# Kernel tuning notes

Measured on AMD Instinct MI355X. Metric: run time of the kernel, lower is better.

Reference implementation:

```python
import jax, jax.numpy as jnp
import numpy as np

B, S, D, H, DH, DF = 8, 1024, 512, 8, 64, 2048
EPS = 1e-5


def layer_norm(x, g, b):
    mu = jnp.mean(x, axis=-1, keepdims=True)
    var = jnp.mean(jnp.square(x - mu), axis=-1, keepdims=True)
    return (x - mu) * jax.lax.rsqrt(var + EPS) * g + b


def rel_shift(x):
    # Transformer-XL relative shift: [b,h,q,k] -> shifted [b,h,q,k]
    b, h, q, k = x.shape
    x = jnp.pad(x, ((0, 0), (0, 0), (0, 0), (1, 0)))
    x = x.reshape(b, h, k + 1, q)[:, :, 1:, :].reshape(b, h, q, k)
    return x


def setup_inputs() -> dict:
    key = jax.random.key(0)
    ks = jax.random.split(key, 16)
    sc = 0.02
    inp = {
        'x': jax.random.normal(ks[0], (B, S, D), jnp.float32),
        'rel_positions': jax.random.normal(ks[1], (S, D), jnp.float32),
        'mask': jnp.triu(jnp.ones((S, S), jnp.bool_), k=1),  # True = masked (causal)
        'Wq': jax.random.normal(ks[2], (D, D), jnp.float32) * sc,
        'Wk': jax.random.normal(ks[3], (D, D), jnp.float32) * sc,
        'Wv': jax.random.normal(ks[4], (D, D), jnp.float32) * sc,
        'Wr': jax.random.normal(ks[5], (D, D), jnp.float32) * sc,
        'Wo': jax.random.normal(ks[6], (D, D), jnp.float32) * sc,
        'u_bias': jax.random.normal(ks[7], (H, DH), jnp.float32) * sc,
        'v_bias': jax.random.normal(ks[8], (H, DH), jnp.float32) * sc,
        'ln1_g': jnp.ones((D,), jnp.float32),
        'ln1_b': jnp.zeros((D,), jnp.float32),
        'W1': jax.random.normal(ks[9], (D, DF), jnp.float32) * sc,
        'b1': jnp.zeros((DF,), jnp.float32),
        'W2': jax.random.normal(ks[10], (DF, D), jnp.float32) * sc,
        'b2': jnp.zeros((D,), jnp.float32),
        'ln2_g': jnp.ones((D,), jnp.float32),
        'ln2_b': jnp.zeros((D,), jnp.float32),
    }
    return inp


def reference(x, rel_positions, mask, Wq, Wk, Wv, Wr, Wo, u_bias, v_bias,
              ln1_g, ln1_b, W1, b1, W2, b2, ln2_g, ln2_b):
    b, s, d = x.shape
    q = (x @ Wq).reshape(b, s, H, DH)
    k = (x @ Wk).reshape(b, s, H, DH)
    v = (x @ Wv).reshape(b, s, H, DH)
    r = (rel_positions @ Wr).reshape(s, H, DH)
    # content term (q + u) k^T and position term (q + v) r^T with rel-shift
    ac = jnp.einsum('bqhd,bkhd->bhqk', q + u_bias, k)
    bd = rel_shift(jnp.einsum('bqhd,khd->bhqk', q + v_bias, r))
    scores = (ac + bd) * (1.0 / np.sqrt(DH))
    scores = jnp.where(mask[None, None, :, :], jnp.asarray(-1e9, scores.dtype), scores)
    attn = jax.nn.softmax(scores, axis=-1)
    ctx = jnp.einsum('bhqk,bkhd->bqhd', attn, v).reshape(b, s, d) @ Wo
    h1 = layer_norm(x + ctx, ln1_g, ln1_b)
    ff = jax.nn.relu(h1 @ W1 + b1) @ W2 + b2
    out = layer_norm(h1 + ff, ln2_g, ln2_b)
    return out, attn
```

## Files before the change

kernel.cpp:

```cpp
#include <hip/hip_runtime.h>
#include <hip/hip_bf16.h>

typedef __hip_bfloat16 bf16;

#define NB 8
#define NS 1024
#define ND 512
#define NH 8
#define NDH 64
#define NDF 2048

typedef __attribute__((ext_vector_type(8))) short s16x8;
typedef __attribute__((ext_vector_type(4))) float f32x4;

__device__ __forceinline__ void storev(float* p, float v) { *p = v; }
__device__ __forceinline__ void storev(bf16* p, float v) { *p = __float2bfloat16(v); }
__device__ __forceinline__ short f2bf(float f) {
    bf16 h = __float2bfloat16(f);
    return *reinterpret_cast<short*>(&h);
}
__device__ __forceinline__ float bf2f(short s) {
    bf16 h = *reinterpret_cast<bf16*>(&s);
    return __bfloat162float(h);
}

__device__ __forceinline__ void gload_lds16(const short* g, short* l) {
    __builtin_amdgcn_global_load_lds(
        (const __attribute__((address_space(1))) unsigned int*)g,
        (__attribute__((address_space(3))) unsigned int*)l, 16, 0, 0);
}

__global__ __launch_bounds__(256) void cast2_kernel(
    const float4* __restrict__ inA, int n4a,
    const float4* __restrict__ inB, int n4b,
    short* __restrict__ outA, short* __restrict__ outB)
{
    int i = blockIdx.x * 256 + threadIdx.x;
    const float4* s; short* d; int j;
    if (i < n4a) { s = inA; d = outA; j = i; }
    else if (i < n4a + n4b) { s = inB; d = outB; j = i - n4a; }
    else return;
    float4 v = s[j];
    short4 o;
    o.x = f2bf(v.x); o.y = f2bf(v.y); o.z = f2bf(v.z); o.w = f2bf(v.w);
    *reinterpret_cast<short4*>(d + (size_t)j * 4) = o;
}

struct TP7 {
    const float* src[7];
    short* dst[7];
    int K[7];
    int N[7];
};

__global__ __launch_bounds__(256) void transpose_cast_all_kernel(TP7 p)
{
    __shared__ float t[32][33];
    const int z = blockIdx.z;
    const float* src = p.src[z];
    short* dst = p.dst[z];
    const int K = p.K[z], N = p.N[z];
    const int ntx = N >> 5;
    const int f = blockIdx.x;
    if (f >= ntx * (K >> 5)) return;
    const int n0 = (f % ntx) * 32, k0 = (f / ntx) * 32;
    const int tx = threadIdx.x & 31, ty = threadIdx.x >> 5;
#pragma unroll
    for (int i = 0; i < 4; ++i)
        t[ty + i * 8][tx] = src[(size_t)(k0 + ty + i * 8) * N + n0 + tx];
    __syncthreads();
#pragma unroll
    for (int i = 0; i < 4; ++i)
        dst[(size_t)(n0 + ty + i * 8) * K + k0 + tx] = f2bf(t[tx][ty + i * 8]);
}

__global__ __launch_bounds__(256) void transpose_v_kernel(
    const short* __restrict__ v, short* __restrict__ vT)
{
    __shared__ short t[32][33];
    const int s0 = blockIdx.x * 32, n0 = blockIdx.y * 32;
    const int bh = blockIdx.z;
    const int h = bh & (NH - 1), b = bh >> 3;
    const int tx = threadIdx.x & 31, ty = threadIdx.x >> 5;
#pragma unroll
    for (int i = 0; i < 4; ++i)
        t[ty + i * 8][tx] = v[(size_t)(b * NS + s0 + ty + i * 8) * ND + h * NDH + n0 + tx];
    __syncthreads();
#pragma unroll
    for (int i = 0; i < 4; ++i)
        vT[((size_t)bh * NDH + n0 + ty + i * 8) * NS + s0 + tx] = t[tx][ty + i * 8];
}

template <typename CT>
__global__ __launch_bounds__(256) void mfma_gemm_kernel(
    const short* __restrict__ A, const short* __restrict__ Bt,
    const float* __restrict__ bias, CT* __restrict__ C,
    int M, int N, int K, int doRelu)
{
    __shared__ __align__(16) short As[128 * 64];
    __shared__ __align__(16) short Bs[128 * 64];
    const int row0 = blockIdx.y * 128;
    const int col0 = blockIdx.x * 128;
    const int tid = threadIdx.x;
    const int lane = tid & 63, w = tid >> 6;
    const int wm = w >> 1, wn = w & 1;
    const int lm = lane & 15, kq = lane >> 4;
    const int srow8 = lane >> 3;
    const int schk8 = lane & 7;

    f32x4 acc[4][4] = {};

    for (int k0 = 0; k0 < K; k0 += 64) {
#pragma unroll
        for (int p = 0; p < 4; ++p) {
            int rbase = p * 32 + w * 8;
            int r = rbase + srow8;
            int gc = schk8 ^ (r & 7);
            gload_lds16(A  + (size_t)(row0 + r) * K + k0 + gc * 8, As + rbase * 64);
            gload_lds16(Bt + (size_t)(col0 + r) * K + k0 + gc * 8, Bs + rbase * 64);
        }
        __syncthreads();

#pragma unroll
        for (int ks = 0; ks < 2; ++ks) {
            s16x8 af[4], bfr[4];
#pragma unroll
            for (int i = 0; i < 4; ++i) {
                int ra = wm * 64 + i * 16 + lm;
                int rb = wn * 64 + i * 16 + lm;
                af[i]  = *reinterpret_cast<const s16x8*>(
                    As + ra * 64 + ((4 * ks + kq) ^ (lm & 7)) * 8);
                bfr[i] = *reinterpret_cast<const s16x8*>(
                    Bs + rb * 64 + ((4 * ks + kq) ^ (lm & 7)) * 8);
            }
#pragma unroll
            for (int i = 0; i < 4; ++i)
#pragma unroll
                for (int j = 0; j < 4; ++j)
                    acc[i][j] = __builtin_amdgcn_mfma_f32_16x16x32_bf16(
                        af[i], bfr[j], acc[i][j], 0, 0, 0);
        }
        __syncthreads();
    }

#pragma unroll
    for (int i = 0; i < 4; ++i) {
        int cr0 = row0 + wm * 64 + i * 16 + kq * 4;
#pragma unroll
        for (int j = 0; j < 4; ++j) {
            int cc = col0 + wn * 64 + j * 16 + lm;
            float bv = bias ? bias[cc] : 0.0f;
#pragma unroll
            for (int r = 0; r < 4; ++r) {
                float v = acc[i][j][r] + bv;
                if (doRelu) v = fmaxf(v, 0.0f);
                storev(&C[(size_t)(cr0 + r) * N + cc], v);
            }
        }
    }
}

template <typename CT>
__global__ __launch_bounds__(256) void mfma_gemm64_kernel(
    const short* __restrict__ A, const short* __restrict__ Bt,
    const float* __restrict__ bias, CT* __restrict__ C,
    int M, int N, int K, int doRelu)
{
    __shared__ __align__(16) short As[2][128 * 64];
    __shared__ __align__(16) short Bs[2][64 * 64];
    const int row0 = blockIdx.y * 128;
    const int col0 = blockIdx.x * 64;
    const int tid = threadIdx.x;
    const int lane = tid & 63, w = tid >> 6;
    const int wm = w >> 1, wn = w & 1;
    const int lm = lane & 15, kq = lane >> 4;
    const int srow8 = lane >> 3;
    const int schk8 = lane & 7;

    f32x4 acc[4][2] = {};

    auto stage = [&](int bufi, int k0) {
#pragma unroll
        for (int p = 0; p < 4; ++p) {
            int rbase = p * 32 + w * 8;
            int r = rbase + srow8;
            int gc = schk8 ^ (r & 7);
            gload_lds16(A + (size_t)(row0 + r) * K + k0 + gc * 8, &As[bufi][rbase * 64]);
        }
#pragma unroll
        for (int p = 0; p < 2; ++p) {
            int rbase = p * 32 + w * 8;
            int r = rbase + srow8;
            int gc = schk8 ^ (r & 7);
            gload_lds16(Bt + (size_t)(col0 + r) * K + k0 + gc * 8, &Bs[bufi][rbase * 64]);
        }
    };

    stage(0, 0);
    __syncthreads();
    int cur = 0;
    for (int k0 = 0; k0 < K; k0 += 64) {
        if (k0 + 64 < K) stage(cur ^ 1, k0 + 64);
#pragma unroll
        for (int ks = 0; ks < 2; ++ks) {
            s16x8 af[4], bfr[2];
#pragma unroll
            for (int i = 0; i < 4; ++i) {
                int ra = wm * 64 + i * 16 + lm;
                af[i] = *reinterpret_cast<const s16x8*>(
                    &As[cur][ra * 64 + ((4 * ks + kq) ^ (lm & 7)) * 8]);
            }
#pragma unroll
            for (int j = 0; j < 2; ++j) {
                int rb = wn * 32 + j * 16 + lm;
                bfr[j] = *reinterpret_cast<const s16x8*>(
                    &Bs[cur][rb * 64 + ((4 * ks + kq) ^ (lm & 7)) * 8]);
            }
#pragma unroll
            for (int i = 0; i < 4; ++i)
#pragma unroll
                for (int j = 0; j < 2; ++j)
                    acc[i][j] = __builtin_amdgcn_mfma_f32_16x16x32_bf16(
                        af[i], bfr[j], acc[i][j], 0, 0, 0);
        }
        __syncthreads();
        cur ^= 1;
    }

#pragma unroll
    for (int i = 0; i < 4; ++i) {
        int cr0 = row0 + wm * 64 + i * 16 + kq * 4;
#pragma unroll
        for (int j = 0; j < 2; ++j) {
            int cc = col0 + wn * 32 + j * 16 + lm;
            float bv = bias ? bias[cc] : 0.0f;
#pragma unroll
            for (int r = 0; r < 4; ++r) {
                float v = acc[i][j][r] + bv;
                if (doRelu) v = fmaxf(v, 0.0f);
                storev(&C[(size_t)(cr0 + r) * N + cc], v);
            }
        }
    }
}

__global__ __launch_bounds__(256) void qkvr_gemm_kernel(
    const short* __restrict__ x_bf, const short* __restrict__ Wqkv,
    const short* __restrict__ rel_bf, const short* __restrict__ WrT,
    const float* __restrict__ ub, const float* __restrict__ vb,
    short* __restrict__ qu, short* __restrict__ qv,
    short* __restrict__ kb, short* __restrict__ vbuf,
    short* __restrict__ r_bf)
{
    const int isRel = blockIdx.x >= 12;
    if (isRel && blockIdx.y >= 8) return;
    const short* A  = isRel ? rel_bf : x_bf;
    const short* Bt = isRel ? WrT : Wqkv;
    const int col0 = isRel ? (blockIdx.x - 12) * 128 : blockIdx.x * 128;
    const int row0 = blockIdx.y * 128;

    __shared__ __align__(16) short As[128 * 64];
    __shared__ __align__(16) short Bs[128 * 64];
    const int tid = threadIdx.x;
    const int lane = tid & 63, w = tid >> 6;
    const int wm = w >> 1, wn = w & 1;
    const int lm = lane & 15, kq = lane >> 4;
    const int srow8 = lane >> 3;
    const int schk8 = lane & 7;

    f32x4 acc[4][4] = {};

    for (int k0 = 0; k0 < ND; k0 += 64) {
#pragma unroll
        for (int p = 0; p < 4; ++p) {
            int rbase = p * 32 + w * 8;
            int r = rbase + srow8;
            int gc = schk8 ^ (r & 7);
            gload_lds16(A  + (size_t)(row0 + r) * ND + k0 + gc * 8, As + rbase * 64);
            gload_lds16(Bt + (size_t)(col0 + r) * ND + k0 + gc * 8, Bs + rbase * 64);
        }
        __syncthreads();

#pragma unroll
        for (int ks = 0; ks < 2; ++ks) {
            s16x8 af[4], bfr[4];
#pragma unroll
            for (int i = 0; i < 4; ++i) {
                int ra = wm * 64 + i * 16 + lm;
                int rb = wn * 64 + i * 16 + lm;
                af[i]  = *reinterpret_cast<const s16x8*>(
                    As + ra * 64 + ((4 * ks + kq) ^ (lm & 7)) * 8);
                bfr[i] = *reinterpret_cast<const s16x8*>(
                    Bs + rb * 64 + ((4 * ks + kq) ^ (lm & 7)) * 8);
            }
#pragma unroll
            for (int i = 0; i < 4; ++i)
#pragma unroll
                for (int j = 0; j < 4; ++j)
                    acc[i][j] = __builtin_amdgcn_mfma_f32_16x16x32_bf16(
                        af[i], bfr[j], acc[i][j], 0, 0, 0);
        }
        __syncthreads();
    }

    const int sec = col0 >> 9;
#pragma unroll
    for (int i = 0; i < 4; ++i) {
        int cr0 = row0 + wm * 64 + i * 16 + kq * 4;
#pragma unroll
        for (int j = 0; j < 4; ++j) {
            int cc = col0 + wn * 64 + j * 16 + lm;
            int c5 = cc & 511;
#pragma unroll
            for (int r = 0; r < 4; ++r) {
                float a = acc[i][j][r];
                size_t idx = (size_t)(cr0 + r) * ND + c5;
                if (isRel) {
                    r_bf[idx] = f2bf(a);
                } else if (sec == 0) {
                    qu[idx] = f2bf(a + ub[c5]);
                    qv[idx] = f2bf(a + vb[c5]);
                } else if (sec == 1) {
                    kb[idx] = f2bf(a);
                } else {
                    vbuf[idx] = f2bf(a);
                }
            }
        }
    }
}

__global__ __launch_bounds__(256) void fused_attn_kernel(
    const short* __restrict__ qu, const short* __restrict__ qv,
    const short* __restrict__ kb, const short* __restrict__ rb,
    const short* __restrict__ vT, float* __restrict__ attn,
    short* __restrict__ ctx)
{
    __shared__ __align__(16) short K_s[64 * 64];
    __shared__ __align__(16) short V_s[64 * 64];
    __shared__ __align__(16) short r_s[2][64 * 64];
    __shared__ __align__(16) short bd_s[64][80];

    const int bid = blockIdx.x;
    const int strip = 15 - (bid >> 6);
    const int bh = bid & 63;
    const int h = bh & (NH - 1), b = bh >> 3;
    const int q0 = strip * 64;
    const int n_kt = strip + 1;
    const int tid = threadIdx.x;
    const int lane = tid & 63, w = tid >> 6;
    const int lm = lane & 15, kq = lane >> 4;
    const int woff = 48 - w * 16;
    const int srow8 = lane >> 3;
    const int schk8 = lane & 7;

    s16x8 aq[2], av[2];
#pragma unroll
    for (int ks = 0; ks < 2; ++ks) {
        const size_t off = (size_t)(b * NS + q0 + w * 16 + lm) * ND + h * NDH + ks * 32 + kq * 8;
        aq[ks] = *reinterpret_cast<const s16x8*>(qu + off);
        av[ks] = *reinterpret_cast<const s16x8*>(qv + off);
    }

    f32x4 apv[4] = {};
    float linv[4];

    for (int pass = 0; pass < 2; ++pass) {
        float lsum[4] = {0.f, 0.f, 0.f, 0.f};
        for (int kt = 0; kt < n_kt; ++kt) {
            const int k0 = kt * 64;
            const int ub0 = k0 - q0 + 960;
            __syncthreads();
#pragma unroll
            for (int p = 0; p < 2; ++p) {
                int rbase = p * 32 + w * 8;
                int grow = rbase + srow8;
                int gc = schk8 ^ (grow & 7);
                gload_lds16(kb + (size_t)(b * NS + k0 + grow) * ND + h * NDH + gc * 8,
                            K_s + rbase * 64);
            }
            if (pass) {
#pragma unroll
                for (int p = 0; p < 2; ++p) {
                    int rbase = p * 32 + w * 8;
                    int grow = rbase + srow8;
                    int gc = schk8 ^ (grow & 7);
                    gload_lds16(vT + ((size_t)bh * NDH + grow) * NS + k0 + gc * 8,
                                V_s + rbase * 64);
                }
            }
            if (kt == 0) {
#pragma unroll
                for (int half = 0; half < 2; ++half)
#pragma unroll
                    for (int p = 0; p < 2; ++p) {
                        int rbase = p * 32 + w * 8;
                        int grow = rbase + srow8;
                        int ur = ub0 + half * 64 + grow; ur = ur > 1023 ? 1023 : ur;
                        int gc = schk8 ^ (grow & 7);
                        gload_lds16(rb + (size_t)ur * ND + h * NDH + gc * 8,
                                    r_s[half] + rbase * 64);
                    }
            } else {
#pragma unroll
                for (int p = 0; p < 2; ++p) {
                    int rbase = p * 32 + w * 8;
                    int grow = rbase + srow8;
                    int ur = ub0 + 64 + grow; ur = ur > 1023 ? 1023 : ur;
                    int gc = schk8 ^ (grow & 7);
                    gload_lds16(rb + (size_t)ur * ND + h * NDH + gc * 8,
                                r_s[(kt + 1) & 1] + rbase * 64);
                }
            }
            __syncthreads();

            f32x4 aac[4] = {};
            f32x4 abd[5] = {};
            __builtin_amdgcn_s_setprio(1);
#pragma unroll
            for (int ks = 0; ks < 2; ++ks) {
#pragma unroll
                for (int j = 0; j < 4; ++j) {
                    int rr = j * 16 + lm;
                    s16x8 bk = *reinterpret_cast<const s16x8*>(
                        K_s + rr * 64 + ((4 * ks + kq) ^ (lm & 7)) * 8);
                    aac[j] = __builtin_amdgcn_mfma_f32_16x16x32_bf16(aq[ks], bk, aac[j], 0, 0, 0);
                }
#pragma unroll
                for (int j = 0; j < 5; ++j) {
                    int rr = woff + j * 16 + lm;
                    const short* rbuf = r_s[(kt + (rr >> 6)) & 1];
                    s16x8 br = *reinterpret_cast<const s16x8*>(
                        rbuf + (rr & 63) * 64 + ((4 * ks + kq) ^ (lm & 7)) * 8);
                    abd[j] = __builtin_amdgcn_mfma_f32_16x16x32_bf16(av[ks], br, abd[j], 0, 0, 0);
                }
            }
            __builtin_amdgcn_s_setprio(0);
#pragma unroll
            for (int j = 0; j < 5; ++j)
#pragma unroll
                for (int r = 0; r < 4; ++r)
                    bd_s[w * 16 + kq * 4 + r][j * 16 + lm] = f2bf(abd[j][r]);

            if (pass == 0) {
#pragma unroll
                for (int jj = 0; jj < 4; ++jj)
#pragma unroll
                    for (int r = 0; r < 4; ++r) {
                        int q_ls = w * 16 + kq * 4 + r;
                        int c = jj * 16 + lm - kq * 4 - r + 15;
                        float s = (aac[jj][r] + bf2f(bd_s[q_ls][c])) * 0.125f;
                        bool ok = (k0 + jj * 16 + lm) <= (q0 + q_ls);
                        lsum[r] += ok ? __expf(s) : 0.0f;
                    }
            } else {
                float sv[4][4];
#pragma unroll
                for (int jj = 0; jj < 4; ++jj)
#pragma unroll
                    for (int r = 0; r < 4; ++r) {
                        int c = jj * 16 + lm - kq * 4 - r + 15;
                        sv[jj][r] = (aac[jj][r] + bf2f(bd_s[w * 16 + kq * 4 + r][c])) * 0.125f;
                    }
                short* ew = &bd_s[w * 16][0];
#pragma unroll
                for (int jj = 0; jj < 4; ++jj)
#pragma unroll
                    for (int r = 0; r < 4; ++r) {
                        int q_ls = w * 16 + kq * 4 + r;
                        int kk = k0 + jj * 16 + lm;
                        bool ok = kk <= (q0 + q_ls);
                        float a = ok ? __expf(sv[jj][r]) * linv[r] : 0.0f;
                        attn[((size_t)bh * NS + q0 + q_ls) * NS + kk] = a;
                        ew[(kq * 4 + r) * 80 + jj * 16 + lm] = f2bf(a);
                    }
#pragma unroll
                for (int ks = 0; ks < 2; ++ks) {
                    s16x8 ae = *reinterpret_cast<const s16x8*>(ew + lm * 80 + ks * 32 + kq * 8);
#pragma unroll
                    for (int jn = 0; jn < 4; ++jn) {
                        s16x8 bv = *reinterpret_cast<const s16x8*>(
                            V_s + (jn * 16 + lm) * 64 + ((4 * ks + kq) ^ (lm & 7)) * 8);
                        apv[jn] = __builtin_amdgcn_mfma_f32_16x16x32_bf16(ae, bv, apv[jn], 0, 0, 0);
                    }
                }
            }
        }
        if (pass == 0) {
#pragma unroll
            for (int r = 0; r < 4; ++r) {
                float v = lsum[r];
                v += __shfl_xor(v, 1); v += __shfl_xor(v, 2);
                v += __shfl_xor(v, 4); v += __shfl_xor(v, 8);
                linv[r] = 1.0f / v;
            }
        }
    }

    const int z = NS - n_kt * 64;
    if (z > 0) {
        const int z4 = z >> 2;
        float4 zz = make_float4(0.f, 0.f, 0.f, 0.f);
        for (int i = tid; i < 64 * z4; i += 256) {
            int zr = i / z4, zc = i - zr * z4;
            *reinterpret_cast<float4*>(
                attn + ((size_t)bh * NS + q0 + zr) * NS + n_kt * 64 + zc * 4) = zz;
        }
    }
#pragma unroll
    for (int jn = 0; jn < 4; ++jn)
#pragma unroll
        for (int r = 0; r < 4; ++r)
            ctx[(size_t)(b * NS + q0 + w * 16 + kq * 4 + r) * ND + h * NDH + jn * 16 + lm] =
                f2bf(apv[jn][r]);
}

__global__ __launch_bounds__(256) void add_ln_kernel(
    const float* __restrict__ xin, const float* __restrict__ yin,
    const float* __restrict__ g, const float* __restrict__ bb,
    float* __restrict__ out, short* __restrict__ out_bf)
{
    __shared__ float red[4];
    __shared__ float red2[4];
    const int row = blockIdx.x;
    const size_t base = (size_t)row * ND;
    const int tid = threadIdx.x;
    const int lane = tid & 63, w = tid >> 6;

    float v0 = xin[base + tid] + yin[base + tid];
    float v1 = xin[base + tid + 256] + yin[base + tid + 256];
    float s = v0 + v1;
#pragma unroll
    for (int o = 32; o > 0; o >>= 1) s += __shfl_xor(s, o);
    if (lane == 0) red[w] = s;
    __syncthreads();
    float mu = (red[0] + red[1] + red[2] + red[3]) * (1.0f / ND);
    float d0 = v0 - mu, d1 = v1 - mu;
    float vs = d0 * d0 + d1 * d1;
#pragma unroll
    for (int o = 32; o > 0; o >>= 1) vs += __shfl_xor(vs, o);
    if (lane == 0) red2[w] = vs;
    __syncthreads();
    float var = (red2[0] + red2[1] + red2[2] + red2[3]) * (1.0f / ND);
    float rs = rsqrtf(var + 1e-5f);
    float o0 = d0 * rs * g[tid] + bb[tid];
    float o1 = d1 * rs * g[tid + 256] + bb[tid + 256];
    out[base + tid] = o0;
    out[base + tid + 256] = o1;
    if (out_bf) {
        out_bf[base + tid] = f2bf(o0);
        out_bf[base + tid + 256] = f2bf(o1);
    }
}

extern "C" void kernel_launch(void* const* d_in, const int* in_sizes, int n_in,
                              void* d_out, int out_size, void* d_ws, size_t ws_size,
                              hipStream_t stream)
{
    const float* x   = (const float*)d_in[0];
    const float* rel = (const float*)d_in[1];
    const float* Wq = (const float*)d_in[3];
    const float* Wk = (const float*)d_in[4];
    const float* Wv = (const float*)d_in[5];
    const float* Wr = (const float*)d_in[6];
    const float* Wo = (const float*)d_in[7];
    const float* ub = (const float*)d_in[8];
    const float* vb = (const float*)d_in[9];
    const float* g1 = (const float*)d_in[10];
    const float* be1 = (const float*)d_in[11];
    const float* W1 = (const float*)d_in[12];
    const float* bb1 = (const float*)d_in[13];
    const float* W2 = (const float*)d_in[14];
    const float* bb2 = (const float*)d_in[15];
    const float* g2 = (const float*)d_in[16];
    const float* be2 = (const float*)d_in[17];

    float* out0 = (float*)d_out;
    float* attn = out0 + (size_t)NB * NS * ND;

    char* ws = (char*)d_ws;
    const size_t SZ_F32 = (size_t)NB * NS * ND * 4;
    const size_t SZ_BF  = (size_t)NB * NS * ND * 2;
    const size_t SZ_MID = (size_t)NB * NS * NDF * 2;
    const size_t SZ_RBF = (size_t)NS * ND * 2;
    const size_t SZ_W   = (size_t)ND * ND * 2;
    const size_t SZ_W12 = (size_t)ND * NDF * 2;
    const size_t needed = 2 * SZ_F32 + 8 * SZ_BF + SZ_MID + 2 * SZ_RBF + 5 * SZ_W + 2 * SZ_W12;
    if (ws_size < needed) return;

    float* tmp  = (float*)ws; ws += SZ_F32;
    float* h1   = (float*)ws; ws += SZ_F32;
    short* x_bf = (short*)ws; ws += SZ_BF;
    short* qu_bf = (short*)ws; ws += SZ_BF;
    short* qv_bf = (short*)ws; ws += SZ_BF;
    short* k_bf = (short*)ws; ws += SZ_BF;
    short* vbuf = (short*)ws; ws += SZ_BF;
    short* vT   = (short*)ws; ws += SZ_BF;
    short* ctx  = (short*)ws; ws += SZ_BF;
    short* h1b  = (short*)ws; ws += SZ_BF;
    short* mid  = (short*)ws; ws += SZ_MID;
    short* rel_bf = (short*)ws; ws += SZ_RBF;
    short* r_bf   = (short*)ws; ws += SZ_RBF;
    short* Wqkv = (short*)ws; ws += 3 * SZ_W;
    short* WrT = (short*)ws; ws += SZ_W;
    short* WoT = (short*)ws; ws += SZ_W;
    short* W1T = (short*)ws; ws += SZ_W12;
    short* W2T = (short*)ws; ws += SZ_W12;

    dim3 blk(256);
    const int M = NB * NS;

    cast2_kernel<<<dim3((M * ND / 4 + NS * ND / 4 + 255) / 256), blk, 0, stream>>>(
        (const float4*)x, M * ND / 4, (const float4*)rel, NS * ND / 4, x_bf, rel_bf);
    TP7 tp;
    tp.src[0] = Wq; tp.dst[0] = Wqkv;                 tp.K[0] = ND;  tp.N[0] = ND;
    tp.src[1] = Wk; tp.dst[1] = Wqkv + (size_t)ND * ND;     tp.K[1] = ND;  tp.N[1] = ND;
    tp.src[2] = Wv; tp.dst[2] = Wqkv + (size_t)2 * ND * ND; tp.K[2] = ND;  tp.N[2] = ND;
    tp.src[3] = Wr; tp.dst[3] = WrT;                  tp.K[3] = ND;  tp.N[3] = ND;
    tp.src[4] = Wo; tp.dst[4] = WoT;                  tp.K[4] = ND;  tp.N[4] = ND;
    tp.src[5] = W1; tp.dst[5] = W1T;                  tp.K[5] = ND;  tp.N[5] = NDF;
    tp.src[6] = W2; tp.dst[6] = W2T;                  tp.K[6] = NDF; tp.N[6] = ND;
    transpose_cast_all_kernel<<<dim3(1024, 1, 7), blk, 0, stream>>>(tp);

    qkvr_gemm_kernel<<<dim3(16, M / 128), blk, 0, stream>>>(
        x_bf, Wqkv, rel_bf, WrT, ub, vb, qu_bf, qv_bf, k_bf, vbuf, r_bf);
    transpose_v_kernel<<<dim3(NS / 32, NDH / 32, NB * NH), blk, 0, stream>>>(vbuf, vT);

    fused_attn_kernel<<<dim3(NB * NH * 16), blk, 0, stream>>>(
        qu_bf, qv_bf, k_bf, r_bf, vT, attn, ctx);

    mfma_gemm64_kernel<float><<<dim3(ND / 64, M / 128), blk, 0, stream>>>(
        ctx, WoT, nullptr, tmp, M, ND, ND, 0);
    add_ln_kernel<<<dim3(M), blk, 0, stream>>>(x, tmp, g1, be1, h1, h1b);

    mfma_gemm_kernel<bf16><<<dim3(NDF / 128, M / 128), blk, 0, stream>>>(
        h1b, W1T, bb1, (bf16*)mid, M, NDF, ND, 1);
    mfma_gemm64_kernel<float><<<dim3(ND / 64, M / 128), blk, 0, stream>>>(
        mid, W2T, bb2, tmp, M, ND, NDF, 0);
    add_ln_kernel<<<dim3(M), blk, 0, stream>>>(h1, tmp, g2, be2, out0, nullptr);
}
```

Before: 293.9 us.

## Double-buffer LDS tiles in GEMM kernels with K-step 32

Both the generic MFMA GEMM and the fused QKV/R projection GEMM now use two LDS buffers of 128x32 tiles. The next K slice is issued via direct global-to-LDS loads while MFMAs run on the current buffer, leaving one barrier per iteration instead of two. The aim is to hide global load latency behind compute. In exchange the K step halves, so there are twice as many iterations and barriers, and the XOR swizzle is adapted to a 4-chunk row layout.

After: 293.1 us. Within noise of the previous version (-0.3%).

```diff
diff --git a/kernel.cpp b/kernel.cpp
--- a/kernel.cpp
+++ b/kernel.cpp
@@ -97,50 +97,53 @@
     const float* __restrict__ bias, CT* __restrict__ C,
     int M, int N, int K, int doRelu)
 {
-    __shared__ __align__(16) short As[128 * 64];
-    __shared__ __align__(16) short Bs[128 * 64];
+    __shared__ __align__(16) short As[2][128 * 32];
+    __shared__ __align__(16) short Bs[2][128 * 32];
     const int row0 = blockIdx.y * 128;
     const int col0 = blockIdx.x * 128;
     const int tid = threadIdx.x;
     const int lane = tid & 63, w = tid >> 6;
     const int wm = w >> 1, wn = w & 1;
     const int lm = lane & 15, kq = lane >> 4;
-    const int srow8 = lane >> 3;
-    const int schk8 = lane & 7;
+    const int srow = lane >> 2;
+    const int schk = lane & 3;
 
     f32x4 acc[4][4] = {};
 
-    for (int k0 = 0; k0 < K; k0 += 64) {
-#pragma unroll
-        for (int p = 0; p < 4; ++p) {
-            int rbase = p * 32 + w * 8;
-            int r = rbase + srow8;
-            int gc = schk8 ^ (r & 7);
-            gload_lds16(A  + (size_t)(row0 + r) * K + k0 + gc * 8, As + rbase * 64);
-            gload_lds16(Bt + (size_t)(col0 + r) * K + k0 + gc * 8, Bs + rbase * 64);
-        }
+    auto stage = [&](int bufi, int k0) {
+#pragma unroll
+        for (int p = 0; p < 2; ++p) {
+            int rbase = p * 64 + w * 16;
+            int r = rbase + srow;
+            int gc = schk ^ ((r >> 1) & 3);
+            gload_lds16(A  + (size_t)(row0 + r) * K + k0 + gc * 8, &As[bufi][rbase * 32]);
+            gload_lds16(Bt + (size_t)(col0 + r) * K + k0 + gc * 8, &Bs[bufi][rbase * 32]);
+        }
+    };
+
+    stage(0, 0);
+    __syncthreads();
+    int cur = 0;
+    for (int k0 = 0; k0 < K; k0 += 32) {
+        if (k0 + 32 < K) stage(cur ^ 1, k0 + 32);
+        s16x8 af[4], bfr[4];
+#pragma unroll
+        for (int i = 0; i < 4; ++i) {
+            int ra = wm * 64 + i * 16 + lm;
+            int rb = wn * 64 + i * 16 + lm;
+            af[i]  = *reinterpret_cast<const s16x8*>(
+                &As[cur][ra * 32 + (kq ^ ((ra >> 1) & 3)) * 8]);
+            bfr[i] = *reinterpret_cast<const s16x8*>(
+                &Bs[cur][rb * 32 + (kq ^ ((rb >> 1) & 3)) * 8]);
+        }
+#pragma unroll
+        for (int i = 0; i < 4; ++i)
+#pragma unroll
+            for (int j = 0; j < 4; ++j)
+                acc[i][j] = __builtin_amdgcn_mfma_f32_16x16x32_bf16(
+                    af[i], bfr[j], acc[i][j], 0, 0, 0);
         __syncthreads();
-
-#pragma unroll
-        for (int ks = 0; ks < 2; ++ks) {
-            s16x8 af[4], bfr[4];
-#pragma unroll
-            for (int i = 0; i < 4; ++i) {
-                int ra = wm * 64 + i * 16 + lm;
-                int rb = wn * 64 + i * 16 + lm;
-                af[i]  = *reinterpret_cast<const s16x8*>(
-                    As + ra * 64 + ((4 * ks + kq) ^ (lm & 7)) * 8);
-                bfr[i] = *reinterpret_cast<const s16x8*>(
-                    Bs + rb * 64 + ((4 * ks + kq) ^ (lm & 7)) * 8);
-            }
-#pragma unroll
-            for (int i = 0; i < 4; ++i)
-#pragma unroll
-                for (int j = 0; j < 4; ++j)
-                    acc[i][j] = __builtin_amdgcn_mfma_f32_16x16x32_bf16(
-                        af[i], bfr[j], acc[i][j], 0, 0, 0);
-        }
-        __syncthreads();
+        cur ^= 1;
     }
 
 #pragma unroll
@@ -259,48 +262,51 @@
     const int col0 = isRel ? (blockIdx.x - 12) * 128 : blockIdx.x * 128;
     const int row0 = blockIdx.y * 128;
 
-    __shared__ __align__(16) short As[128 * 64];
-    __shared__ __align__(16) short Bs[128 * 64];
+    __shared__ __align__(16) short As[2][128 * 32];
+    __shared__ __align__(16) short Bs[2][128 * 32];
     const int tid = threadIdx.x;
     const int lane = tid & 63, w = tid >> 6;
     const int wm = w >> 1, wn = w & 1;
     const int lm = lane & 15, kq = lane >> 4;
-    const int srow8 = lane >> 3;
-    const int schk8 = lane & 7;
+    const int srow = lane >> 2;
+    const int schk = lane & 3;
 
     f32x4 acc[4][4] = {};
 
-    for (int k0 = 0; k0 < ND; k0 += 64) {
-#pragma unroll
-        for (int p = 0; p < 4; ++p) {
-            int rbase = p * 32 + w * 8;
-            int r = rbase + srow8;
-            int gc = schk8 ^ (r & 7);
-            gload_lds16(A  + (size_t)(row0 + r) * ND + k0 + gc * 8, As + rbase * 64);
-            gload_lds16(Bt + (size_t)(col0 + r) * ND + k0 + gc * 8, Bs + rbase * 64);
-        }
+    auto stage = [&](int bufi, int k0) {
+#pragma unroll
+        for (int p = 0; p < 2; ++p) {
+            int rbase = p * 64 + w * 16;
+            int r = rbase + srow;
+            int gc = schk ^ ((r >> 1) & 3);
+            gload_lds16(A  + (size_t)(row0 + r) * ND + k0 + gc * 8, &As[bufi][rbase * 32]);
+            gload_lds16(Bt + (size_t)(col0 + r) * ND + k0 + gc * 8, &Bs[bufi][rbase * 32]);
+        }
+    };
+
+    stage(0, 0);
+    __syncthreads();
+    int cur = 0;
+    for (int k0 = 0; k0 < ND; k0 += 32) {
+        if (k0 + 32 < ND) stage(cur ^ 1, k0 + 32);
+        s16x8 af[4], bfr[4];
+#pragma unroll
+        for (int i = 0; i < 4; ++i) {
+            int ra = wm * 64 + i * 16 + lm;
+            int rb = wn * 64 + i * 16 + lm;
+            af[i]  = *reinterpret_cast<const s16x8*>(
+                &As[cur][ra * 32 + (kq ^ ((ra >> 1) & 3)) * 8]);
+            bfr[i] = *reinterpret_cast<const s16x8*>(
+                &Bs[cur][rb * 32 + (kq ^ ((rb >> 1) & 3)) * 8]);
+        }
+#pragma unroll
+        for (int i = 0; i < 4; ++i)
+#pragma unroll
+            for (int j = 0; j < 4; ++j)
+                acc[i][j] = __builtin_amdgcn_mfma_f32_16x16x32_bf16(
+                    af[i], bfr[j], acc[i][j], 0, 0, 0);
         __syncthreads();
-
-#pragma unroll
-        for (int ks = 0; ks < 2; ++ks) {
-            s16x8 af[4], bfr[4];
-#pragma unroll
-            for (int i = 0; i < 4; ++i) {
-                int ra = wm * 64 + i * 16 + lm;
-                int rb = wn * 64 + i * 16 + lm;
-                af[i]  = *reinterpret_cast<const s16x8*>(
-                    As + ra * 64 + ((4 * ks + kq) ^ (lm & 7)) * 8);
-                bfr[i] = *reinterpret_cast<const s16x8*>(
-                    Bs + rb * 64 + ((4 * ks + kq) ^ (lm & 7)) * 8);
-            }
-#pragma unroll
-            for (int i = 0; i < 4; ++i)
-#pragma unroll
-                for (int j = 0; j < 4; ++j)
-                    acc[i][j] = __builtin_amdgcn_mfma_f32_16x16x32_bf16(
-                        af[i], bfr[j], acc[i][j], 0, 0, 0);
-        }
-        __syncthreads();
+        cur ^= 1;
     }
 
     const int sec = col0 >> 9;
```
